# Kernel optimization log

Hardware: AMD Instinct MI355X
Metric: run time of the kernel (lower is better)

## Reference

```python
import jax, jax.numpy as jnp
import numpy as np

N = 50000      # nodes
E = 800000     # edges
D_IN, D_HID, D_OUT = 1433, 64, 7
EPS = 1e-7       # eps[float32] in hgcn Hyperboloid
MIN_NORM = 1e-15
MAX_NORM = 1e6
# c = 1 -> K = 1/c = 1, sqrtK = 1 (folded into constants below)


def proj(x):
    # reset time coordinate so point lies on the hyperboloid
    y = x[:, 1:]
    y_sqnorm = jnp.sum(y * y, axis=1, keepdims=True)
    x0 = jnp.sqrt(jnp.clip(1.0 + y_sqnorm, EPS))
    return jnp.concatenate([x0, y], axis=1)


def proj_tan0(u):
    return jnp.concatenate([jnp.zeros_like(u[:, :1]), u[:, 1:]], axis=1)


def expmap0(u):
    x = u[:, 1:]
    x_norm = jnp.clip(jnp.linalg.norm(x, axis=1, keepdims=True), MIN_NORM)
    theta = x_norm
    res = jnp.concatenate([jnp.cosh(theta), jnp.sinh(theta) * x / x_norm], axis=1)
    return proj(res)


def logmap0(x):
    y = x[:, 1:]
    y_norm = jnp.clip(jnp.linalg.norm(y, axis=1, keepdims=True), MIN_NORM)
    theta = jnp.clip(x[:, :1], 1.0 + EPS)
    return jnp.concatenate([jnp.zeros_like(theta), jnp.arccosh(theta) * y / y_norm], axis=1)


def minkowski_dot(x, y):
    return jnp.sum(x * y, axis=-1, keepdims=True) - 2.0 * x[:, :1] * y[:, :1]


def proj_tan(u, x):
    ux = jnp.sum(x[:, 1:] * u[:, 1:], axis=1, keepdims=True)
    v0 = ux / jnp.clip(x[:, :1], EPS)
    return jnp.concatenate([v0, u[:, 1:]], axis=1)


def expmap(u, x):
    normu = jnp.sqrt(jnp.clip(minkowski_dot(u, u), EPS))
    normu = jnp.minimum(normu, MAX_NORM)
    theta = jnp.clip(normu, MIN_NORM)
    result = jnp.cosh(theta) * x + jnp.sinh(theta) * u / theta
    return proj(result)


def ptransp0(x, u):
    x0, y = x[:, :1], x[:, 1:]
    y_norm = jnp.clip(jnp.linalg.norm(y, axis=1, keepdims=True), MIN_NORM)
    yn = y / y_norm
    v = jnp.concatenate([-y_norm, (1.0 - x0) * yn], axis=1)
    alpha = jnp.sum(yn * u[:, 1:], axis=1, keepdims=True)
    return proj_tan(u - alpha * v, x)


def mobius_add(x, y):
    u = logmap0(y)
    v = ptransp0(x, u)
    return expmap(v, x)


def hyp_linear(x, W, b):
    # mobius_matvec then hyperbolic bias add (dropout=0)
    mv = expmap0(logmap0(x) @ W.T)
    res = proj(mv)
    hyp_bias = proj(expmap0(proj_tan0(b[None, :])))
    return proj(mobius_add(res, hyp_bias))


def hyp_agg(x, row, col, edge_weight):
    # spmm(adj, logmap0(x)) via edge-list scatter-add
    xt = logmap0(x)
    msg = edge_weight[:, None] * xt[col]          # [E, d]
    support = jax.ops.segment_sum(msg, row, num_segments=N)
    return proj(expmap0(support))


def hyp_act(x):
    xt = jax.nn.relu(logmap0(x))
    xt = proj_tan0(xt)
    return proj(expmap0(xt))


def setup_inputs() -> dict:
    key = jax.random.key(0)
    ks = jax.random.split(key, 8)
    return {
        "x": jax.random.normal(ks[0], (N, D_IN), dtype=jnp.float32),
        "row": jax.random.randint(ks[1], (E,), 0, N),
        "col": jax.random.randint(ks[2], (E,), 0, N),
        "edge_weight": jax.random.uniform(ks[3], (E,), dtype=jnp.float32) * 0.1,
        "W1": jax.random.normal(ks[4], (D_HID, D_IN), dtype=jnp.float32) * 0.02,
        "b1": jax.random.normal(ks[5], (D_HID,), dtype=jnp.float32) * 0.02,
        "W2": jax.random.normal(ks[6], (D_OUT, D_HID), dtype=jnp.float32) * 0.05,
        "b2": jax.random.normal(ks[7], (D_OUT,), dtype=jnp.float32) * 0.02,
    }


def reference(x, row, col, edge_weight, W1, b1, W2, b2):
    # map features to the hyperboloid
    x_hyp = proj(expmap0(proj_tan0(x)))
    # layer 1: HypLinear -> HypAgg -> HypAct
    h = hyp_act(hyp_agg(hyp_linear(x_hyp, W1, b1), row, col, edge_weight))
    # layer 2
    h = hyp_act(hyp_agg(hyp_linear(h, W2, b2), row, col, edge_weight))
    # back to tangent space at origin
    return proj_tan0(logmap0(h))
```

## Files before the change

kernel.cpp:

```cpp
#include <hip/hip_runtime.h>
#include <hip/hip_bf16.h>

#define NN 50000
#define EE 800000
#define DIN 1433
#define KTOT 1432
#define KHALF 716
#define NKT 23
#define NB 196
#define EPSC 1e-7f
#define MINN 1e-15f
#define MAXN 1e6f

typedef __attribute__((ext_vector_type(8))) short bf16x8;
typedef __attribute__((ext_vector_type(4))) float f32x4;

#define WF_OFF     0
#define Z1A_OFF    94208
#define Z1B_OFF    (Z1A_OFF + 3200000)
#define XT3_OFF    (Z1B_OFF + 3200000)
#define CNT_OFF    (XT3_OFF + 400000)
#define ROWPTR_OFF (CNT_OFF + 50000)
#define CUR_OFF    (ROWPTR_OFF + 50002)
#define BSUM_OFF   (CUR_OFF + 50000)
#define BOFF_OFF   (BSUM_OFF + 256)
#define UB_OFF     (BOFF_OFF + 256)
#define EP_OFF     (UB_OFF + 128)

__device__ __forceinline__ float wsum(float v) {
#pragma unroll
  for (int o = 1; o < 64; o <<= 1) v += __shfl_xor(v, o, 64);
  return v;
}

__device__ __forceinline__ float gsum8(float v) {
#pragma unroll
  for (int o = 1; o < 8; o <<= 1) v += __shfl_xor(v, o, 64);
  return v;
}

__device__ __forceinline__ void split_bf(float v, unsigned int& hbits16, unsigned int& lbits16) {
  unsigned int b = __float_as_uint(v);
  unsigned int hb = b & 0xFFFF0000u;
  float r = v - __uint_as_float(hb);
  unsigned int lb = __float_as_uint(r);
  lbits16 = (lb + 0x7FFFu + ((lb >> 16) & 1u)) >> 16;
  hbits16 = hb >> 16;
}

__device__ __forceinline__ float fsinh(float x) {
  float e = __expf(x);
  return 0.5f * (e - __fdividef(1.f, e));
}
__device__ __forceinline__ float facoshp(float z) {
  return __logf(z + sqrtf(fmaxf(z * z - 1.f, 0.f)));
}

__device__ float bias_tangent(const float* b, int lane, int D) {
  const bool sp = (lane >= 1) && (lane < D);
  float bsp = sp ? b[lane] : 0.f;
  float rb = fmaxf(sqrtf(wsum(bsp * bsp)), MINN);
  float bsh = fsinh(rb);
  float hb = sp ? bsh * __fdividef(bsp, rb) : 0.f;
  float hbn2 = wsum(hb * hb);
  float hb0 = sqrtf(fmaxf(1.f + hbn2, EPSC));
  float hbyn = fmaxf(sqrtf(hbn2), MINN);
  return sp ? facoshp(fmaxf(hb0, 1.f + EPSC)) * __fdividef(hb, hbyn) : 0.f;
}

__device__ float chain_with_u(float z, float u, int lane, int D) {
  const bool sp = (lane >= 1) && (lane < D);
  float s = sp ? z : 0.f;
  float r = fmaxf(sqrtf(wsum(s * s)), MINN);
  float sh = fsinh(r);
  float y = sp ? sh * __fdividef(s, r) : 0.f;
  float yn2 = wsum(y * y);
  float x0 = sqrtf(fmaxf(1.f + yn2, EPSC));
  float y_norm = fmaxf(sqrtf(yn2), MINN);
  float ynv = sp ? __fdividef(y, y_norm) : 0.f;
  float alpha = wsum(ynv * u);
  float wsp = sp ? u - alpha * (1.f - x0) * ynv : 0.f;
  float ux = wsum(y * wsp);
  float v0 = __fdividef(ux, fmaxf(x0, EPSC));
  float vt = (lane == 0) ? v0 : wsp;
  float md = wsum(vt * vt) - 2.f * v0 * v0;
  float nu = sqrtf(fmaxf(md, EPSC));
  nu = fminf(nu, MAXN);
  float th = fmaxf(nu, MINN);
  float e = __expf(th), ei = __fdividef(1.f, e);
  float cth = 0.5f * (e + ei), sth = 0.5f * (e - ei);
  float resx = (lane == 0) ? x0 : y;
  float eres = fmaf(cth, resx, sth * __fdividef(vt, th));
  float en2 = wsum(sp ? eres * eres : 0.f);
  float e0 = sqrtf(fmaxf(1.f + en2, EPSC));
  float eyn = fmaxf(sqrtf(en2), MINN);
  return sp ? facoshp(fmaxf(e0, 1.f + EPSC)) * __fdividef(eres, eyn) : 0.f;
}

__device__ float agg_act_chain(float sin_, int lane, int D) {
  const bool sp = (lane >= 1) && (lane < D);
  float s = sp ? sin_ : 0.f;
  float r = fmaxf(sqrtf(wsum(s * s)), MINN);
  float sh = fsinh(r);
  float g = sp ? sh * __fdividef(s, r) : 0.f;
  float gn2 = wsum(g * g);
  float g0 = sqrtf(fmaxf(1.f + gn2, EPSC));
  float gyn = fmaxf(sqrtf(gn2), MINN);
  float l = sp ? facoshp(fmaxf(g0, 1.f + EPSC)) * __fdividef(g, gyn) : 0.f;
  float t = fmaxf(l, 0.f);
  float rt = fmaxf(sqrtf(wsum(t * t)), MINN);
  float sht = fsinh(rt);
  float h = sp ? sht * __fdividef(t, rt) : 0.f;
  float hn2 = wsum(h * h);
  float h0 = sqrtf(fmaxf(1.f + hn2, EPSC));
  float hyn = fmaxf(sqrtf(hn2), MINN);
  return sp ? facoshp(fmaxf(h0, 1.f + EPSC)) * __fdividef(h, hyn) : 0.f;
}

__device__ float agg_act_chain8(float sin_, int f) {
  const bool sp = (f >= 1) && (f < 7);
  float s = sp ? sin_ : 0.f;
  float r = fmaxf(sqrtf(gsum8(s * s)), MINN);
  float sh = fsinh(r);
  float g = sp ? sh * __fdividef(s, r) : 0.f;
  float gn2 = gsum8(g * g);
  float g0 = sqrtf(fmaxf(1.f + gn2, EPSC));
  float gyn = fmaxf(sqrtf(gn2), MINN);
  float l = sp ? facoshp(fmaxf(g0, 1.f + EPSC)) * __fdividef(g, gyn) : 0.f;
  float t = fmaxf(l, 0.f);
  float rt = fmaxf(sqrtf(gsum8(t * t)), MINN);
  float sht = fsinh(rt);
  float h = sp ? sht * __fdividef(t, rt) : 0.f;
  float hn2 = gsum8(h * h);
  float h0 = sqrtf(fmaxf(1.f + hn2, EPSC));
  float hyn = fmaxf(sqrtf(hn2), MINN);
  return sp ? facoshp(fmaxf(h0, 1.f + EPSC)) * __fdividef(h, hyn) : 0.f;
}

__global__ __launch_bounds__(256) void prep_wb(const float* __restrict__ W1,
                                               const float* __restrict__ b1,
                                               const float* __restrict__ b2,
                                               unsigned short* __restrict__ wfrag,
                                               float* __restrict__ ub) {
  if (blockIdx.x == 92) {
    const int w = threadIdx.x >> 6, lane = threadIdx.x & 63;
    if (w == 0) ub[lane] = bias_tangent(b1, lane, 64);
    else if (w == 1) ub[64 + lane] = bias_tangent(b2, lane, 7);
    return;
  }
  int idx = blockIdx.x * 256 + threadIdx.x;
  if (idx >= 2 * NKT * 8 * 64) return;
  int lane = idx & 63;
  int c = (idx >> 6) & 7;
  int rest = idx >> 9;
  int kt = rest % NKT;
  int half = rest / NKT;
  int type = c >> 2, nt = c & 3;
  int col = nt * 16 + (lane & 15);
  unsigned short vals[8];
#pragma unroll
  for (int i = 0; i < 8; ++i) {
    int lk = kt * 32 + (lane >> 4) * 8 + i;
    float wv = (lk < KHALF) ? W1[col * DIN + half * KHALF + lk + 1] : 0.f;
    unsigned int h16, l16;
    split_bf(wv, h16, l16);
    vals[i] = (unsigned short)((type == 0) ? h16 : l16);
  }
  unsigned short* dst = wfrag + (((size_t)(half * NKT + kt) * 8 + c) * 64 + lane) * 8;
#pragma unroll
  for (int i = 0; i < 8; ++i) dst[i] = vals[i];
}

__global__ __launch_bounds__(256) void gemm_half(const float* __restrict__ x,
                                                 const unsigned short* __restrict__ wfrag,
                                                 float* __restrict__ z) {
  __shared__ __align__(16) float XA[3 * 1024];
  __shared__ __align__(16) unsigned short BB[2][8][64][8];
  const int tid = threadIdx.x;
  const int w = tid >> 6, lane = tid & 63;
  const int row0 = blockIdx.x * 32;
  const int half = blockIdx.y;
  const unsigned short* wf = wfrag + (size_t)half * NKT * 4096;
  float* zp = z + (size_t)half * 3200000;
  const int nt0 = (w >> 1) * 2;

  auto stageB = [&](int kt, int p) {
    const unsigned short* src = wf + (size_t)kt * 4096 + (2 * w) * 512 + lane * 8;
    __builtin_amdgcn_global_load_lds(
        (const __attribute__((address_space(1))) unsigned int*)src,
        (__attribute__((address_space(3))) unsigned int*)(&BB[p][2 * w][0][0]), 16, 0, 0);
    __builtin_amdgcn_global_load_lds(
        (const __attribute__((address_space(1))) unsigned int*)(src + 512),
        (__attribute__((address_space(3))) unsigned int*)(&BB[p][2 * w + 1][0][0]), 16, 0, 0);
  };
  auto stageA = [&](int kt, int q) {
    const int r = w * 8 + (lane >> 3);
    const int lb = (lane & 7) ^ (r & 7);
    int grow = row0 + r; if (grow >= NN) grow = NN - 1;
    size_t off = (size_t)grow * DIN + 1 + half * KHALF + kt * 32 + lb * 4;
    if (off > (size_t)NN * DIN - 4) off = (size_t)NN * DIN - 4;
    __builtin_amdgcn_global_load_lds(
        (const __attribute__((address_space(1))) unsigned int*)(x + off),
        (__attribute__((address_space(3))) unsigned int*)(XA + q * 1024 + w * 256),
        16, 0, 0);
  };

  f32x4 acc[2];
  acc[0] = (f32x4){0.f, 0.f, 0.f, 0.f};
  acc[1] = (f32x4){0.f, 0.f, 0.f, 0.f};

  stageB(0, 0);
  stageA(0, 0);
  stageA(1, 1);
  __builtin_amdgcn_sched_barrier(0);
  asm volatile("s_waitcnt vmcnt(1)" ::: "memory");
  __builtin_amdgcn_s_barrier();
  __builtin_amdgcn_sched_barrier(0);

  const int rr = (w & 1) * 16 + (lane & 15);
  const int b0 = (lane >> 4) * 2;
  const int pb0 = (b0 ^ (rr & 7)) * 4;
  const int pb1 = ((b0 + 1) ^ (rr & 7)) * 4;

  for (int kt = 0; kt < NKT; ++kt) {
    if (kt + 1 < NKT) stageB(kt + 1, (kt + 1) & 1);
    if (kt + 2 < NKT) stageA(kt + 2, (kt + 2) % 3);
    const float* xa = XA + (kt % 3) * 1024 + rr * 32;
    float4 f0 = *(const float4*)(xa + pb0);
    float4 f1 = *(const float4*)(xa + pb1);
    float af[8] = {f0.x, f0.y, f0.z, f0.w, f1.x, f1.y, f1.z, f1.w};
    unsigned int h[8], l[8];
#pragma unroll
    for (int j = 0; j < 8; ++j) split_bf(af[j], h[j], l[j]);
    bf16x8 ah, al;
#pragma unroll
    for (int j = 0; j < 8; ++j) { ah[j] = (short)h[j]; al[j] = (short)l[j]; }
    bf16x8 bh[2], bl[2];
#pragma unroll
    for (int n = 0; n < 2; ++n) {
      bh[n] = *(const bf16x8*)&BB[kt & 1][nt0 + n][lane][0];
      bl[n] = *(const bf16x8*)&BB[kt & 1][4 + nt0 + n][lane][0];
    }
#pragma unroll
    for (int n = 0; n < 2; ++n) {
      acc[n] = __builtin_amdgcn_mfma_f32_16x16x32_bf16(ah, bh[n], acc[n], 0, 0, 0);
      acc[n] = __builtin_amdgcn_mfma_f32_16x16x32_bf16(ah, bl[n], acc[n], 0, 0, 0);
      acc[n] = __builtin_amdgcn_mfma_f32_16x16x32_bf16(al, bh[n], acc[n], 0, 0, 0);
    }
    if (kt + 1 < NKT) {
      __builtin_amdgcn_sched_barrier(0);
      asm volatile("s_waitcnt lgkmcnt(0)" ::: "memory");
      if (kt + 2 < NKT) asm volatile("s_waitcnt vmcnt(1)" ::: "memory");
      else              asm volatile("s_waitcnt vmcnt(0)" ::: "memory");
      __builtin_amdgcn_s_barrier();
      __builtin_amdgcn_sched_barrier(0);
    }
  }
#pragma unroll
  for (int n = 0; n < 2; ++n)
#pragma unroll
    for (int i = 0; i < 4; ++i) {
      int orow = row0 + (w & 1) * 16 + (lane >> 4) * 4 + i;
      int ocol = (nt0 + n) * 16 + (lane & 15);
      if (orow < NN) zp[(size_t)orow * 64 + ocol] = acc[n][i];
    }
}

__global__ __launch_bounds__(256) void node1(const float* __restrict__ z1a,
                                             const float* __restrict__ z1b,
                                             const float* __restrict__ ub, float* xt) {
  const int node = blockIdx.x * 4 + (threadIdx.x >> 6);
  const int lane = threadIdx.x & 63;
  const int idx = node * 64 + lane;
  float z = z1a[idx] + z1b[idx];
  float u1 = ub[lane];
  float o = chain_with_u(z, u1, lane, 64);
  xt[idx] = o;
}

__global__ __launch_bounds__(256) void k_zero(int* __restrict__ cnt) {
  int i = blockIdx.x * 256 + threadIdx.x;
  if (i < NN) cnt[i] = 0;
}

__global__ __launch_bounds__(256) void k_hist(const int* __restrict__ row, int* __restrict__ cnt) {
  int e = blockIdx.x * 256 + threadIdx.x;
  if (e < EE) atomicAdd(&cnt[row[e]], 1);
}

__global__ __launch_bounds__(256) void k_blocksum(const int* __restrict__ cnt,
                                                  int* __restrict__ bsum) {
  __shared__ int wpart[4];
  int i = blockIdx.x * 256 + threadIdx.x;
  int v = (i < NN) ? cnt[i] : 0;
  int s = v;
#pragma unroll
  for (int o = 1; o < 64; o <<= 1) s += __shfl_xor(s, o, 64);
  if ((threadIdx.x & 63) == 0) wpart[threadIdx.x >> 6] = s;
  __syncthreads();
  if (threadIdx.x == 0) bsum[blockIdx.x] = wpart[0] + wpart[1] + wpart[2] + wpart[3];
}

__global__ __launch_bounds__(256) void k_scanb(const int* __restrict__ bsum,
                                               int* __restrict__ boff) {
  __shared__ int s[256];
  int t = threadIdx.x;
  int v = (t < NB) ? bsum[t] : 0;
  s[t] = v;
  __syncthreads();
  for (int o = 1; o < 256; o <<= 1) {
    int a = (t >= o) ? s[t - o] : 0;
    __syncthreads();
    s[t] += a;
    __syncthreads();
  }
  if (t < NB) boff[t] = s[t] - v;
}

__global__ __launch_bounds__(256) void k_apply(const int* __restrict__ cnt,
                                               const int* __restrict__ boff,
                                               int* __restrict__ rowptr, int* __restrict__ cur) {
  __shared__ int s[256];
  int i = blockIdx.x * 256 + threadIdx.x;
  int t = threadIdx.x;
  int v = (i < NN) ? cnt[i] : 0;
  s[t] = v;
  __syncthreads();
  for (int o = 1; o < 256; o <<= 1) {
    int a = (t >= o) ? s[t - o] : 0;
    __syncthreads();
    s[t] += a;
    __syncthreads();
  }
  int ex = s[t] - v + boff[blockIdx.x];
  if (i < NN) { rowptr[i] = ex; cur[i] = ex; }
  if (i == NN - 1) rowptr[NN] = EE;
}

__global__ __launch_bounds__(256) void k_scatter(const int* __restrict__ row,
                                                 const int* __restrict__ col,
                                                 const float* __restrict__ ew,
                                                 int* __restrict__ cur, uint2* __restrict__ ep) {
  int e = blockIdx.x * 256 + threadIdx.x;
  if (e < EE) {
    int p = atomicAdd(&cur[row[e]], 1);
    uint2 q;
    q.x = (unsigned int)col[e];
    q.y = __float_as_uint(ew[e]);
    ep[p] = q;
  }
}

__global__ __launch_bounds__(256) void agg1_node2(const int* __restrict__ rowptr,
                                                  const uint2* __restrict__ ep,
                                                  const float* __restrict__ xt,
                                                  const float* __restrict__ W2,
                                                  const float* __restrict__ ub,
                                                  float* __restrict__ xt3) {
  const int node = blockIdx.x * 4 + (threadIdx.x >> 6);
  const int lane = threadIdx.x & 63;
  const int s0 = rowptr[node], s1 = rowptr[node + 1];
  float a0 = 0.f, a1 = 0.f, a2 = 0.f, a3 = 0.f;
  float a4 = 0.f, a5 = 0.f, a6 = 0.f, a7 = 0.f;
  int p = s0;
  for (; p + 8 <= s1; p += 8) {
    uint2 q0 = ep[p], q1 = ep[p + 1], q2 = ep[p + 2], q3 = ep[p + 3];
    uint2 q4 = ep[p + 4], q5 = ep[p + 5], q6 = ep[p + 6], q7 = ep[p + 7];
    a0 = fmaf(__uint_as_float(q0.y), xt[(size_t)q0.x * 64 + lane], a0);
    a1 = fmaf(__uint_as_float(q1.y), xt[(size_t)q1.x * 64 + lane], a1);
    a2 = fmaf(__uint_as_float(q2.y), xt[(size_t)q2.x * 64 + lane], a2);
    a3 = fmaf(__uint_as_float(q3.y), xt[(size_t)q3.x * 64 + lane], a3);
    a4 = fmaf(__uint_as_float(q4.y), xt[(size_t)q4.x * 64 + lane], a4);
    a5 = fmaf(__uint_as_float(q5.y), xt[(size_t)q5.x * 64 + lane], a5);
    a6 = fmaf(__uint_as_float(q6.y), xt[(size_t)q6.x * 64 + lane], a6);
    a7 = fmaf(__uint_as_float(q7.y), xt[(size_t)q7.x * 64 + lane], a7);
  }
  for (; p < s1; ++p) {
    uint2 q = ep[p];
    a0 = fmaf(__uint_as_float(q.y), xt[(size_t)q.x * 64 + lane], a0);
  }
  float acc = ((a0 + a1) + (a2 + a3)) + ((a4 + a5) + (a6 + a7));
  float xt2 = agg_act_chain(acc, lane, 64);
  float z2 = 0.f;
#pragma unroll
  for (int jj = 1; jj < 7; ++jj) {
    float wv = W2[jj * 64 + lane];
    float sjj = wsum(xt2 * wv);
    if (lane == jj) z2 = sjj;
  }
  float u2 = ub[64 + lane];
  float o = chain_with_u(z2, u2, lane, 7);
  if (lane < 8) xt3[node * 8 + lane] = o;
}

__global__ __launch_bounds__(256) void agg2_final(const int* __restrict__ rowptr,
                                                  const uint2* __restrict__ ep,
                                                  const float* __restrict__ xt3,
                                                  float* __restrict__ out) {
  const int node = blockIdx.x * 32 + (threadIdx.x >> 3);
  const int f = threadIdx.x & 7;
  const int nc = (node < NN) ? node : (NN - 1);
  const int s0 = rowptr[nc], s1 = rowptr[nc + 1];
  float a0 = 0.f, a1 = 0.f, a2 = 0.f, a3 = 0.f;
  int p = s0;
  for (; p + 4 <= s1; p += 4) {
    uint2 q0 = ep[p], q1 = ep[p + 1], q2 = ep[p + 2], q3 = ep[p + 3];
    a0 = fmaf(__uint_as_float(q0.y), xt3[(size_t)q0.x * 8 + f], a0);
    a1 = fmaf(__uint_as_float(q1.y), xt3[(size_t)q1.x * 8 + f], a1);
    a2 = fmaf(__uint_as_float(q2.y), xt3[(size_t)q2.x * 8 + f], a2);
    a3 = fmaf(__uint_as_float(q3.y), xt3[(size_t)q3.x * 8 + f], a3);
  }
  for (; p < s1; ++p) {
    uint2 q = ep[p];
    a0 = fmaf(__uint_as_float(q.y), xt3[(size_t)q.x * 8 + f], a0);
  }
  float acc = (a0 + a1) + (a2 + a3);
  float o = agg_act_chain8(acc, f);
  if (node < NN && f < 7) out[node * 7 + f] = o;
}

extern "C" void kernel_launch(void* const* d_in, const int* in_sizes, int n_in,
                              void* d_out, int out_size, void* d_ws, size_t ws_size,
                              hipStream_t stream) {
  const float* x = (const float*)d_in[0];
  const int* row = (const int*)d_in[1];
  const int* col = (const int*)d_in[2];
  const float* ew = (const float*)d_in[3];
  const float* W1 = (const float*)d_in[4];
  const float* b1 = (const float*)d_in[5];
  const float* W2 = (const float*)d_in[6];
  const float* b2 = (const float*)d_in[7];
  float* ws = (float*)d_ws;
  unsigned short* wfrag = (unsigned short*)(ws + WF_OFF);
  float* z1a = ws + Z1A_OFF;
  float* z1b = ws + Z1B_OFF;
  float* xt3 = ws + XT3_OFF;
  int* cnt = (int*)(ws + CNT_OFF);
  int* rowptr = (int*)(ws + ROWPTR_OFF);
  int* cur = (int*)(ws + CUR_OFF);
  int* bsum = (int*)(ws + BSUM_OFF);
  int* boff = (int*)(ws + BOFF_OFF);
  float* ub = ws + UB_OFF;
  uint2* ep = (uint2*)(ws + EP_OFF);
  float* out = (float*)d_out;

  k_zero<<<dim3(NB), dim3(256), 0, stream>>>(cnt);
  k_hist<<<dim3(3125), dim3(256), 0, stream>>>(row, cnt);
  k_blocksum<<<dim3(NB), dim3(256), 0, stream>>>(cnt, bsum);
  k_scanb<<<dim3(1), dim3(256), 0, stream>>>(bsum, boff);
  k_apply<<<dim3(NB), dim3(256), 0, stream>>>(cnt, boff, rowptr, cur);
  k_scatter<<<dim3(3125), dim3(256), 0, stream>>>(row, col, ew, cur, ep);

  prep_wb<<<dim3(93), dim3(256), 0, stream>>>(W1, b1, b2, wfrag, ub);
  gemm_half<<<dim3(1563, 2), dim3(256), 0, stream>>>(x, wfrag, z1a);
  node1<<<dim3(12500), dim3(256), 0, stream>>>(z1a, z1b, ub, z1a);

  agg1_node2<<<dim3(12500), dim3(256), 0, stream>>>(rowptr, ep, z1a, W2, ub, xt3);
  agg2_final<<<dim3(1563), dim3(256), 0, stream>>>(rowptr, ep, xt3, out);
}
```

Before: 303.2 us.

## Fuse CSR construction into one cooperative kernel and fold zeroing into prep

Replaces the five CSR-building kernels (histogram, block sums, block scan, apply, scatter) with one cooperative kernel that separates the phases with grid-wide syncs. The counter zeroing moves into extra blocks of the weight-prep kernel. This targets per-launch overhead and inter-kernel gaps, in exchange for grid.sync costs and a fixed 1024-block grid-stride loop over the edges.

```diff
diff --git a/kernel.cpp b/kernel.cpp
--- a/kernel.cpp
+++ b/kernel.cpp
@@ -1,5 +1,8 @@
 #include <hip/hip_runtime.h>
 #include <hip/hip_bf16.h>
+#include <hip/hip_cooperative_groups.h>
+
+namespace cg = cooperative_groups;
 
 #define NN 50000
 #define EE 800000
@@ -137,11 +140,17 @@
   return sp ? facoshp(fmaxf(h0, 1.f + EPSC)) * __fdividef(h, hyn) : 0.f;
 }
 
-__global__ __launch_bounds__(256) void prep_wb(const float* __restrict__ W1,
-                                               const float* __restrict__ b1,
-                                               const float* __restrict__ b2,
-                                               unsigned short* __restrict__ wfrag,
-                                               float* __restrict__ ub) {
+__global__ __launch_bounds__(256) void prep_wb_zero(const float* __restrict__ W1,
+                                                    const float* __restrict__ b1,
+                                                    const float* __restrict__ b2,
+                                                    unsigned short* __restrict__ wfrag,
+                                                    float* __restrict__ ub,
+                                                    int* __restrict__ cnt) {
+  if (blockIdx.x >= 93) {
+    int i = (blockIdx.x - 93) * 256 + threadIdx.x;
+    if (i < NN) cnt[i] = 0;
+    return;
+  }
   if (blockIdx.x == 92) {
     const int w = threadIdx.x >> 6, lane = threadIdx.x & 63;
     if (w == 0) ub[lane] = bias_tangent(b1, lane, 64);
@@ -149,7 +158,6 @@
     return;
   }
   int idx = blockIdx.x * 256 + threadIdx.x;
-  if (idx >= 2 * NKT * 8 * 64) return;
   int lane = idx & 63;
   int c = (idx >> 6) & 7;
   int rest = idx >> 9;
@@ -169,6 +177,71 @@
   unsigned short* dst = wfrag + (((size_t)(half * NKT + kt) * 8 + c) * 64 + lane) * 8;
 #pragma unroll
   for (int i = 0; i < 8; ++i) dst[i] = vals[i];
+}
+
+__global__ __launch_bounds__(256) void csr_coop(const int* __restrict__ row,
+                                                const int* __restrict__ col,
+                                                const float* __restrict__ ew,
+                                                int* __restrict__ cnt,
+                                                int* __restrict__ rowptr,
+                                                int* __restrict__ cur,
+                                                int* __restrict__ bsum,
+                                                int* __restrict__ boff,
+                                                uint2* __restrict__ ep) {
+  cg::grid_group grid = cg::this_grid();
+  __shared__ int sh[256];
+  const int nth = gridDim.x * 256;
+  const int gtid = blockIdx.x * 256 + threadIdx.x;
+  const int t = threadIdx.x;
+  for (int e = gtid; e < EE; e += nth) atomicAdd(&cnt[row[e]], 1);
+  grid.sync();
+  if (blockIdx.x < NB) {
+    int i = blockIdx.x * 256 + t;
+    int v = (i < NN) ? cnt[i] : 0;
+    int s = v;
+#pragma unroll
+    for (int o = 1; o < 64; o <<= 1) s += __shfl_xor(s, o, 64);
+    if ((t & 63) == 0) sh[t >> 6] = s;
+    __syncthreads();
+    if (t == 0) bsum[blockIdx.x] = sh[0] + sh[1] + sh[2] + sh[3];
+  }
+  grid.sync();
+  if (blockIdx.x == 0) {
+    int v = (t < NB) ? bsum[t] : 0;
+    sh[t] = v;
+    __syncthreads();
+    for (int o = 1; o < 256; o <<= 1) {
+      int a = (t >= o) ? sh[t - o] : 0;
+      __syncthreads();
+      sh[t] += a;
+      __syncthreads();
+    }
+    if (t < NB) boff[t] = sh[t] - v;
+  }
+  grid.sync();
+  if (blockIdx.x < NB) {
+    int i = blockIdx.x * 256 + t;
+    int v = (i < NN) ? cnt[i] : 0;
+    sh[t] = v;
+    __syncthreads();
+    for (int o = 1; o < 256; o <<= 1) {
+      int a = (t >= o) ? sh[t - o] : 0;
+      __syncthreads();
+      sh[t] += a;
+      __syncthreads();
+    }
+    int ex = sh[t] - v + boff[blockIdx.x];
+    if (i < NN) { rowptr[i] = ex; cur[i] = ex; }
+    if (i == NN - 1) rowptr[NN] = EE;
+  }
+  grid.sync();
+  for (int e = gtid; e < EE; e += nth) {
+    int p = atomicAdd(&cur[row[e]], 1);
+    uint2 q;
+    q.x = (unsigned int)col[e];
+    q.y = __float_as_uint(ew[e]);
+    ep[p] = q;
+  }
 }
 
 __global__ __launch_bounds__(256) void gemm_half(const float* __restrict__ x,
@@ -276,79 +349,6 @@
   float u1 = ub[lane];
   float o = chain_with_u(z, u1, lane, 64);
   xt[idx] = o;
-}
-
-__global__ __launch_bounds__(256) void k_zero(int* __restrict__ cnt) {
-  int i = blockIdx.x * 256 + threadIdx.x;
-  if (i < NN) cnt[i] = 0;
-}
-
-__global__ __launch_bounds__(256) void k_hist(const int* __restrict__ row, int* __restrict__ cnt) {
-  int e = blockIdx.x * 256 + threadIdx.x;
-  if (e < EE) atomicAdd(&cnt[row[e]], 1);
-}
-
-__global__ __launch_bounds__(256) void k_blocksum(const int* __restrict__ cnt,
-                                                  int* __restrict__ bsum) {
-  __shared__ int wpart[4];
-  int i = blockIdx.x * 256 + threadIdx.x;
-  int v = (i < NN) ? cnt[i] : 0;
-  int s = v;
-#pragma unroll
-  for (int o = 1; o < 64; o <<= 1) s += __shfl_xor(s, o, 64);
-  if ((threadIdx.x & 63) == 0) wpart[threadIdx.x >> 6] = s;
-  __syncthreads();
-  if (threadIdx.x == 0) bsum[blockIdx.x] = wpart[0] + wpart[1] + wpart[2] + wpart[3];
-}
-
-__global__ __launch_bounds__(256) void k_scanb(const int* __restrict__ bsum,
-                                               int* __restrict__ boff) {
-  __shared__ int s[256];
-  int t = threadIdx.x;
-  int v = (t < NB) ? bsum[t] : 0;
-  s[t] = v;
-  __syncthreads();
-  for (int o = 1; o < 256; o <<= 1) {
-    int a = (t >= o) ? s[t - o] : 0;
-    __syncthreads();
-    s[t] += a;
-    __syncthreads();
-  }
-  if (t < NB) boff[t] = s[t] - v;
-}
-
-__global__ __launch_bounds__(256) void k_apply(const int* __restrict__ cnt,
-                                               const int* __restrict__ boff,
-                                               int* __restrict__ rowptr, int* __restrict__ cur) {
-  __shared__ int s[256];
-  int i = blockIdx.x * 256 + threadIdx.x;
-  int t = threadIdx.x;
-  int v = (i < NN) ? cnt[i] : 0;
-  s[t] = v;
-  __syncthreads();
-  for (int o = 1; o < 256; o <<= 1) {
-    int a = (t >= o) ? s[t - o] : 0;
-    __syncthreads();
-    s[t] += a;
-    __syncthreads();
-  }
-  int ex = s[t] - v + boff[blockIdx.x];
-  if (i < NN) { rowptr[i] = ex; cur[i] = ex; }
-  if (i == NN - 1) rowptr[NN] = EE;
-}
-
-__global__ __launch_bounds__(256) void k_scatter(const int* __restrict__ row,
-                                                 const int* __restrict__ col,
-                                                 const float* __restrict__ ew,
-                                                 int* __restrict__ cur, uint2* __restrict__ ep) {
-  int e = blockIdx.x * 256 + threadIdx.x;
-  if (e < EE) {
-    int p = atomicAdd(&cur[row[e]], 1);
-    uint2 q;
-    q.x = (unsigned int)col[e];
-    q.y = __float_as_uint(ew[e]);
-    ep[p] = q;
-  }
 }
 
 __global__ __launch_bounds__(256) void agg1_node2(const int* __restrict__ rowptr,
@@ -444,14 +444,15 @@
   uint2* ep = (uint2*)(ws + EP_OFF);
   float* out = (float*)d_out;
 
-  k_zero<<<dim3(NB), dim3(256), 0, stream>>>(cnt);
-  k_hist<<<dim3(3125), dim3(256), 0, stream>>>(row, cnt);
-  k_blocksum<<<dim3(NB), dim3(256), 0, stream>>>(cnt, bsum);
-  k_scanb<<<dim3(1), dim3(256), 0, stream>>>(bsum, boff);
-  k_apply<<<dim3(NB), dim3(256), 0, stream>>>(cnt, boff, rowptr, cur);
-  k_scatter<<<dim3(3125), dim3(256), 0, stream>>>(row, col, ew, cur, ep);
-
-  prep_wb<<<dim3(93), dim3(256), 0, stream>>>(W1, b1, b2, wfrag, ub);
+  prep_wb_zero<<<dim3(289), dim3(256), 0, stream>>>(W1, b1, b2, wfrag, ub, cnt);
+
+  {
+    void* kargs[] = {(void*)&row, (void*)&col, (void*)&ew, (void*)&cnt,
+                     (void*)&rowptr, (void*)&cur, (void*)&bsum, (void*)&boff,
+                     (void*)&ep};
+    hipLaunchCooperativeKernel((void*)csr_coop, dim3(1024), dim3(256), kargs, 0, stream);
+  }
+
   gemm_half<<<dim3(1563, 2), dim3(256), 0, stream>>>(x, wfrag, z1a);
   node1<<<dim3(12500), dim3(256), 0, stream>>>(z1a, z1b, ub, z1a);
 
```

Measured after the change: 705.9 us. 133% more time.
